# Performance work log

Hardware: AMD Instinct MI355X
Metric: run time of the kernel (lower is better)

The kernel has to match this reference:

```python
import jax, jax.numpy as jnp
import numpy as np

N_NODES = 100000
N_EDGES = 1600000
N_GRAPHS = 256
IN_DIM, HID = 30, 40

def setup_inputs() -> dict:
    key = jax.random.key(0)
    ks = jax.random.split(key, 12)
    x = jax.random.normal(ks[0], (N_NODES, IN_DIM), dtype=jnp.float32)
    edge_index = jax.random.randint(ks[1], (2, N_EDGES), 0, N_NODES, dtype=jnp.int64)
    batch = jnp.sort(jax.random.randint(ks[2], (N_NODES,), 0, N_GRAPHS, dtype=jnp.int64))
    def glorot(k, shape):
        lim = float(np.sqrt(6.0 / (shape[0] + shape[1])))
        return jax.random.uniform(k, shape, dtype=jnp.float32, minval=-lim, maxval=lim)
    return {
        'x': x, 'edge_index': edge_index, 'batch': batch,
        'W1': glorot(ks[3], (IN_DIM, HID)), 'b1': jnp.zeros((HID,), jnp.float32),
        'W2': glorot(ks[4], (HID, HID)),    'b2': jnp.zeros((HID,), jnp.float32),
        'W3': glorot(ks[5], (HID, HID)),    'b3': jnp.zeros((HID,), jnp.float32),
        'lin_w': glorot(ks[6], (HID, 1)),   'lin_b': jnp.zeros((1,), jnp.float32),
    }

def _gcn_layer(x, src, dst, norm, W, b, n_nodes):
    # x: [N, Fin] -> [N, Fout]; fused gather-matmul-scatter form of GCNConv
    h = x @ W                                   # dense transform first (Fout small)
    msg = h[src] * norm[:, None]                # [E+N, Fout] gather + edge scale
    out = jax.ops.segment_sum(msg, dst, num_segments=n_nodes)
    return out + b

def reference(x, edge_index, batch, W1, b1, W2, b2, W3, b3, lin_w, lin_b):
    n = x.shape[0]
    loops = jnp.arange(n, dtype=edge_index.dtype)
    src = jnp.concatenate([edge_index[0], loops])  # add self loops (GCNConv default)
    dst = jnp.concatenate([edge_index[1], loops])
    deg = jax.ops.segment_sum(jnp.ones_like(dst, dtype=x.dtype), dst, num_segments=n)
    dinv = jax.lax.rsqrt(jnp.maximum(deg, 1.0))    # deg >= 1 thanks to self loops
    norm = dinv[src] * dinv[dst]

    h = jax.nn.relu(_gcn_layer(x, src, dst, norm, W1, b1, n))  # dropout inactive (eval)
    h = jax.nn.relu(_gcn_layer(h, src, dst, norm, W2, b2, n))
    h = jax.nn.relu(_gcn_layer(h, src, dst, norm, W3, b3, n))

    # global_mean_pool over graphs
    g_sum = jax.ops.segment_sum(h, batch, num_segments=N_GRAPHS)
    cnt = jax.ops.segment_sum(jnp.ones((n,), h.dtype), batch, num_segments=N_GRAPHS)
    g = g_sum / jnp.maximum(cnt, 1.0)[:, None]
    return g @ lin_w + lin_b                      # [N_GRAPHS, 1]
```

## Files before the change

kernel.cpp:

```cpp
#include <hip/hip_runtime.h>

#define HID 40
#define RBKT 196
#define BSH 9
#define CAP 12288
#define EPB 4096


__device__ inline unsigned pack2_bf16(float a, float b) {
    unsigned ua = __float_as_uint(a);
    unsigned ub = __float_as_uint(b);
    ua = (ua + 0x7fffu + ((ua >> 16) & 1u)) >> 16;
    ub = (ub + 0x7fffu + ((ub >> 16) & 1u)) & 0xffff0000u;
    return ua | ub;
}

__device__ inline void acc8_bf16(float* acc, uint4 v) {
    acc[0] += __uint_as_float(v.x << 16);
    acc[1] += __uint_as_float(v.x & 0xffff0000u);
    acc[2] += __uint_as_float(v.y << 16);
    acc[3] += __uint_as_float(v.y & 0xffff0000u);
    acc[4] += __uint_as_float(v.z << 16);
    acc[5] += __uint_as_float(v.z & 0xffff0000u);
    acc[6] += __uint_as_float(v.w << 16);
    acc[7] += __uint_as_float(v.w & 0xffff0000u);
}

__global__ void clear_kernel(int* __restrict__ bucket_cnt, float* __restrict__ g_sum, int G) {
    int t = blockIdx.x * blockDim.x + threadIdx.x;
    if (t < RBKT) bucket_cnt[t] = 0;
    if (t < G) g_sum[t] = 0.f;
}


__global__ __launch_bounds__(256) void binA_kernel(
        const int* __restrict__ esrc, const int* __restrict__ edst, int E,
        int* __restrict__ bucket_cnt, int* __restrict__ bucket_data) {
    __shared__ int cnt_l[RBKT];
    __shared__ int base_l[RBKT];
    int t = threadIdx.x;
    for (int b = t; b < RBKT; b += 256) cnt_l[b] = 0;
    __syncthreads();
    int e0 = blockIdx.x * EPB;
    int e1 = min(e0 + EPB, E);
    for (int e = e0 + t; e < e1; e += 256) {
        atomicAdd(&cnt_l[edst[e] >> BSH], 1);
    }
    __syncthreads();
    for (int b = t; b < RBKT; b += 256) {
        int c = cnt_l[b];
        base_l[b] = (c > 0) ? atomicAdd(&bucket_cnt[b], c) : 0;
        cnt_l[b] = 0;
    }
    __syncthreads();
    for (int e = e0 + t; e < e1; e += 256) {
        int d = edst[e];
        int s = esrc[e];
        int b = d >> BSH;
        int off = base_l[b] + atomicAdd(&cnt_l[b], 1);
        if (off < CAP) bucket_data[(size_t)b * CAP + off] = (s << BSH) | (d & 511);
    }
}

__global__ void scan_buckets_kernel(const int* __restrict__ cnt, int* __restrict__ base) {
    __shared__ int s[256];
    int t = threadIdx.x;
    int c = (t < RBKT) ? min(cnt[t], CAP) : 0;
    s[t] = c;
    __syncthreads();
    for (int off = 1; off < 256; off <<= 1) {
        int y = (t >= off) ? s[t - off] : 0;
        __syncthreads();
        s[t] += y;
        __syncthreads();
    }
    if (t < RBKT) base[t] = s[t] - c;
    if (t == RBKT - 1) base[RBKT] = s[t];
}

__global__ __launch_bounds__(256) void buildB_kernel(
        const int* __restrict__ bucket_cnt, const int* __restrict__ bucket_base,
        const int* __restrict__ bucket_data,
        int* __restrict__ rowptr, int* __restrict__ mid, int* __restrict__ csr,
        float* __restrict__ dinv, int n, int half) {
    __shared__ int deg_l[512];
    __shared__ int deg_lo[512];
    __shared__ int off_lo[512];
    __shared__ int off_hi[512];
    __shared__ int ps[256];
    int r = blockIdx.x;
    int t = threadIdx.x;
    int cnt = min(bucket_cnt[r], CAP);
    int base = bucket_base[r];
    int node0 = r << BSH;
    int nr = min(512, n - node0);
    for (int i = t; i < 512; i += 256) { deg_l[i] = 0; deg_lo[i] = 0; }
    __syncthreads();
    const int* data = bucket_data + (size_t)r * CAP;
    for (int e = t; e < cnt; e += 256) {
        int v = data[e];
        atomicAdd(&deg_l[v & 511], 1);
        if ((v >> BSH) < half) atomicAdd(&deg_lo[v & 511], 1);
    }
    __syncthreads();
    int a0 = deg_l[2 * t], a1 = deg_l[2 * t + 1];
    ps[t] = a0 + a1;
    __syncthreads();
    for (int off = 1; off < 256; off <<= 1) {
        int y = (t >= off) ? ps[t - off] : 0;
        __syncthreads();
        ps[t] += y;
        __syncthreads();
    }
    int excl = ps[t] - (a0 + a1);
    off_lo[2 * t] = excl;
    off_lo[2 * t + 1] = excl + a0;
    off_hi[2 * t] = excl + deg_lo[2 * t];
    off_hi[2 * t + 1] = excl + a0 + deg_lo[2 * t + 1];
    __syncthreads();
    for (int i = t; i < nr; i += 256) {
        int rp = base + off_lo[i];
        rowptr[node0 + i] = rp;
        mid[node0 + i] = rp + deg_lo[i];
        dinv[node0 + i] = rsqrtf((float)(deg_l[i] + 1));
    }
    if (r == RBKT - 1 && t == 0) rowptr[n] = base + cnt;
    __syncthreads();
    for (int e = t; e < cnt; e += 256) {
        int v = data[e];
        int s = v >> BSH;
        int d = v & 511;
        int p = (s < half) ? atomicAdd(&off_lo[d], 1) : atomicAdd(&off_hi[d], 1);
        csr[base + p] = s;
    }
}


__global__ __launch_bounds__(256) void scale_bf16_kernel(
        const float* __restrict__ x, const float* __restrict__ dinv,
        unsigned* __restrict__ xs, int n) {
    int t = blockIdx.x * blockDim.x + threadIdx.x;
    int i = t >> 4, p = t & 15;
    if (i >= n) return;
    float a = 0.f, b = 0.f;
    if (p < 15) {
        float d = dinv[i];
        a = x[i * 30 + 2 * p] * d;
        b = x[i * 30 + 2 * p + 1] * d;
    }
    xs[(size_t)i * 16 + p] = pack2_bf16(a, b);
}

template <int TPN>
__global__ __launch_bounds__(256) void gather_bf16_kernel(
        const unsigned* __restrict__ xs, const int* __restrict__ rowptr,
        const int* __restrict__ mid, const int* __restrict__ csr,
        const float* __restrict__ dinv, unsigned* __restrict__ gout, int n) {
    int t = blockIdx.x * blockDim.x + threadIdx.x;
    int i = t / TPN;
    int q = t - i * TPN;
    if (i >= n) return;
    const uint4* tab = reinterpret_cast<const uint4*>(xs);
    float acc[8];
    {
        uint4 v = tab[(size_t)i * TPN + q];
        acc[0] = __uint_as_float(v.x << 16);
        acc[1] = __uint_as_float(v.x & 0xffff0000u);
        acc[2] = __uint_as_float(v.y << 16);
        acc[3] = __uint_as_float(v.y & 0xffff0000u);
        acc[4] = __uint_as_float(v.z << 16);
        acc[5] = __uint_as_float(v.z & 0xffff0000u);
        acc[6] = __uint_as_float(v.w << 16);
        acc[7] = __uint_as_float(v.w & 0xffff0000u);
    }
    int e0 = rowptr[i], m = mid[i], e1 = rowptr[i + 1];
    int e = e0;
    for (; e + 4 <= m; e += 4) {
        int s0 = csr[e], s1 = csr[e + 1], s2 = csr[e + 2], s3 = csr[e + 3];
        uint4 v0 = tab[(size_t)s0 * TPN + q];
        uint4 v1 = tab[(size_t)s1 * TPN + q];
        uint4 v2 = tab[(size_t)s2 * TPN + q];
        uint4 v3 = tab[(size_t)s3 * TPN + q];
        acc8_bf16(acc, v0);
        acc8_bf16(acc, v1);
        acc8_bf16(acc, v2);
        acc8_bf16(acc, v3);
    }
    for (; e < m; e++) acc8_bf16(acc, tab[(size_t)csr[e] * TPN + q]);
    for (; e + 4 <= e1; e += 4) {
        int s0 = csr[e], s1 = csr[e + 1], s2 = csr[e + 2], s3 = csr[e + 3];
        uint4 v0 = tab[(size_t)s0 * TPN + q];
        uint4 v1 = tab[(size_t)s1 * TPN + q];
        uint4 v2 = tab[(size_t)s2 * TPN + q];
        uint4 v3 = tab[(size_t)s3 * TPN + q];
        acc8_bf16(acc, v0);
        acc8_bf16(acc, v1);
        acc8_bf16(acc, v2);
        acc8_bf16(acc, v3);
    }
    for (; e < e1; e++) acc8_bf16(acc, tab[(size_t)csr[e] * TPN + q]);
    float d = dinv[i];
    uint4 o;
    o.x = pack2_bf16(acc[0] * d, acc[1] * d);
    o.y = pack2_bf16(acc[2] * d, acc[3] * d);
    o.z = pack2_bf16(acc[4] * d, acc[5] * d);
    o.w = pack2_bf16(acc[6] * d, acc[7] * d);
    reinterpret_cast<uint4*>(gout)[(size_t)i * TPN + q] = o;
}

template <int INF, int RU, bool POOL>
__global__ __launch_bounds__(256) void transform_bf16_kernel(
        const unsigned* __restrict__ tin, const float* __restrict__ W,
        const float* __restrict__ bias, const float* __restrict__ dinv,
        const float* __restrict__ lin_w, const int* __restrict__ batch,
        unsigned* __restrict__ out, float* __restrict__ g_sum, int n) {
    constexpr int OUTF = 40;
    constexpr int OPF  = 10;
    __shared__ float Ws[INF * OUTF];
    __shared__ unsigned tile[64 * (RU + 1)];
    __shared__ float lw[POOL ? OUTF : 1];
    __shared__ float sarr[POOL ? 256 : 1];
    const int tid = threadIdx.x;
    for (int t = tid; t < INF * OUTF; t += 256) Ws[t] = W[t];
    if (POOL && tid < OUTF) lw[tid] = lin_w[tid];
    const int base = blockIdx.x * 64;
    const unsigned* g = tin + (size_t)base * RU;
    const int limit = (n - base) * RU;
    for (int idx = tid; idx < 64 * RU; idx += 256) {
        if (idx < limit) {
            int row = idx / RU, col = idx - row * RU;
            tile[row * (RU + 1) + col] = g[idx];
        }
    }
    __syncthreads();
    const int node_l = tid >> 2, q = tid & 3;
    const int node = base + node_l;
    const bool valid = (node < n);
    if (POOL) sarr[tid] = 0.f;
    if (valid) {
        const unsigned* myrow = &tile[node_l * (RU + 1)];
        float acc[OPF];
        #pragma unroll
        for (int j = 0; j < OPF; j++) acc[j] = 0.f;
        #pragma unroll
        for (int k2 = 0; k2 < INF / 2; k2++) {
            unsigned u = myrow[k2];
            float x0 = __uint_as_float(u << 16);
            float x1 = __uint_as_float(u & 0xffff0000u);
            const float* w0 = &Ws[(2 * k2) * OUTF + q * OPF];
            const float* w1 = &Ws[(2 * k2 + 1) * OUTF + q * OPF];
            #pragma unroll
            for (int j = 0; j < OPF; j++) acc[j] += x0 * w0[j];
            #pragma unroll
            for (int j = 0; j < OPF; j++) acc[j] += x1 * w1[j];
        }
        if (!POOL) {
            float d = dinv[node];
            unsigned* orow = out + (size_t)node * 20 + q * 5;
            #pragma unroll
            for (int j = 0; j < 5; j++) {
                int f = q * OPF + 2 * j;
                float v0 = fmaxf(acc[2 * j] + bias[f], 0.f) * d;
                float v1 = fmaxf(acc[2 * j + 1] + bias[f + 1], 0.f) * d;
                orow[j] = pack2_bf16(v0, v1);
            }
        } else {
            float s = 0.f;
            #pragma unroll
            for (int j = 0; j < OPF; j++) {
                int f = q * OPF + j;
                s += fmaxf(acc[j] + bias[f], 0.f) * lw[f];
            }
            sarr[tid] = s;
        }
    }
    if (POOL) {
        __syncthreads();
        if (tid < 64) {
            float s = sarr[tid * 4] + sarr[tid * 4 + 1] + sarr[tid * 4 + 2] + sarr[tid * 4 + 3];
            int node2 = base + tid;
            bool v2 = (node2 < n);
            int gg = batch[v2 ? node2 : (n - 1)];
            if (!v2) s = 0.f;
            int g0 = __shfl(gg, 0, 64);
            if (__all(gg == g0)) {
                #pragma unroll
                for (int off = 32; off > 0; off >>= 1) s += __shfl_xor(s, off, 64);
                if (tid == 0) atomicAdd(&g_sum[g0], s);
            } else {
                if (v2) atomicAdd(&g_sum[gg], s);
            }
        }
    }
}

__global__ void finalize_kernel(const float* __restrict__ g_sum,
                                const int* __restrict__ batch,
                                const float* __restrict__ lin_b,
                                float* __restrict__ out, int n, int G) {
    int b = blockIdx.x * blockDim.x + threadIdx.x;
    if (b >= G) return;
    int lo = 0, hi = n;
    while (lo < hi) { int m = (lo + hi) >> 1; if (batch[m] < b) lo = m + 1; else hi = m; }
    int lo2 = lo, hi2 = n;
    while (lo2 < hi2) { int m = (lo2 + hi2) >> 1; if (batch[m] < b + 1) lo2 = m + 1; else hi2 = m; }
    int cnt = lo2 - lo;
    out[b] = g_sum[b] / (float)(cnt > 0 ? cnt : 1) + lin_b[0];
}


static inline size_t align_up(size_t v, size_t a) { return (v + a - 1) / a * a; }

extern "C" void kernel_launch(void* const* d_in, const int* in_sizes, int n_in,
                              void* d_out, int out_size, void* d_ws, size_t ws_size,
                              hipStream_t stream) {
    const float* x      = (const float*)d_in[0];
    const int*   esrc   = (const int*)d_in[1];
    const int*   batch  = (const int*)d_in[2];
    const float* W1     = (const float*)d_in[3];
    const float* b1     = (const float*)d_in[4];
    const float* W2     = (const float*)d_in[5];
    const float* b2     = (const float*)d_in[6];
    const float* W3     = (const float*)d_in[7];
    const float* b3     = (const float*)d_in[8];
    const float* lin_w  = (const float*)d_in[9];
    const float* lin_b  = (const float*)d_in[10];
    float* out = (float*)d_out;

    const int n = in_sizes[0] / 30;
    const int E = in_sizes[1] / 2;
    const int G = out_size;
    const int* edst = esrc + E;

    char* w = (char*)d_ws;
    size_t off = 0;
    auto take = [&](size_t bytes) { size_t o = off; off = align_up(off + bytes, 256); return (void*)(w + o); };
    int*      bucket_cnt  = (int*)take((size_t)RBKT * 4);
    int*      bucket_base = (int*)take((size_t)(RBKT + 1) * 4);
    int*      rowptr      = (int*)take((size_t)(n + 1) * 4);
    int*      mid         = (int*)take((size_t)n * 4);
    float*    dinv        = (float*)take((size_t)n * 4);
    int*      csr         = (int*)take((size_t)E * 4);
    float*    g_sum       = (float*)take((size_t)G * 4);
    size_t bd = (size_t)RBKT * CAP * 4;
    size_t x1 = (size_t)n * 16 * 4;
    void* shared_region = take(bd > x1 ? bd : x1);
    int*      bucket_data = (int*)shared_region;
    unsigned* xs1         = (unsigned*)shared_region;
    unsigned* agg         = (unsigned*)take((size_t)n * 20 * 4);
    unsigned* tbA         = (unsigned*)take((size_t)n * 20 * 4);
    unsigned* tbB         = (unsigned*)take((size_t)n * 20 * 4);
    (void)ws_size;

    clear_kernel<<<1, 256, 0, stream>>>(bucket_cnt, g_sum, G);

    binA_kernel<<<(E + EPB - 1) / EPB, 256, 0, stream>>>(esrc, edst, E, bucket_cnt, bucket_data);
    scan_buckets_kernel<<<1, 256, 0, stream>>>(bucket_cnt, bucket_base);
    buildB_kernel<<<RBKT, 256, 0, stream>>>(bucket_cnt, bucket_base, bucket_data,
                                            rowptr, mid, csr, dinv, n, n / 2);

    int nblk64 = (n + 63) / 64;

    scale_bf16_kernel<<<((size_t)n * 16 + 255) / 256, 256, 0, stream>>>(x, dinv, xs1, n);
    gather_bf16_kernel<4><<<((size_t)n * 4 + 255) / 256, 256, 0, stream>>>(
        xs1, rowptr, mid, csr, dinv, agg, n);
    transform_bf16_kernel<30, 16, false><<<nblk64, 256, 0, stream>>>(
        agg, W1, b1, dinv, nullptr, nullptr, tbA, nullptr, n);
    gather_bf16_kernel<5><<<((size_t)n * 5 + 255) / 256, 256, 0, stream>>>(
        tbA, rowptr, mid, csr, dinv, agg, n);
    transform_bf16_kernel<40, 20, false><<<nblk64, 256, 0, stream>>>(
        agg, W2, b2, dinv, nullptr, nullptr, tbB, nullptr, n);
    gather_bf16_kernel<5><<<((size_t)n * 5 + 255) / 256, 256, 0, stream>>>(
        tbB, rowptr, mid, csr, dinv, agg, n);
    transform_bf16_kernel<40, 20, true><<<nblk64, 256, 0, stream>>>(
        agg, W3, b3, dinv, lin_w, batch, nullptr, g_sum, n);

    finalize_kernel<<<1, 256, 0, stream>>>(g_sum, batch, lin_b, out, n, G);
}
```

Before: 216.6 us.

## Restructure transform kernel to one node per thread with output-slice blocks

The dense transform kernel now gives each thread a whole node and half of the output features (20), splitting the two output halves across paired blocks of 256 nodes. Weights are read directly from global memory (uniform across the wavefront, so scalar/broadcast loads) instead of staging them in shared memory, and the pooling reduction uses per-wavefront shuffles without a shared-memory pass. This cuts shared-memory weight traffic and block-level syncs. In exchange each input tile is loaded twice (once per slice), register pressure rises, and the inner k loop is no longer forced to unroll.

```diff
diff --git a/kernel.cpp b/kernel.cpp
--- a/kernel.cpp
+++ b/kernel.cpp
@@ -209,46 +209,42 @@
 }
 
 template <int INF, int RU, bool POOL>
-__global__ __launch_bounds__(256) void transform_bf16_kernel(
+__global__ __launch_bounds__(256) void transform_v2_kernel(
         const unsigned* __restrict__ tin, const float* __restrict__ W,
         const float* __restrict__ bias, const float* __restrict__ dinv,
         const float* __restrict__ lin_w, const int* __restrict__ batch,
         unsigned* __restrict__ out, float* __restrict__ g_sum, int n) {
     constexpr int OUTF = 40;
-    constexpr int OPF  = 10;
-    __shared__ float Ws[INF * OUTF];
-    __shared__ unsigned tile[64 * (RU + 1)];
-    __shared__ float lw[POOL ? OUTF : 1];
-    __shared__ float sarr[POOL ? 256 : 1];
+    constexpr int OPF  = 20;
+    __shared__ unsigned tile[256 * (RU + 1)];
     const int tid = threadIdx.x;
-    for (int t = tid; t < INF * OUTF; t += 256) Ws[t] = W[t];
-    if (POOL && tid < OUTF) lw[tid] = lin_w[tid];
-    const int base = blockIdx.x * 64;
+    const int nodeblk = blockIdx.x >> 1;
+    const int slice = blockIdx.x & 1;
+    const int q0 = slice * OPF;
+    const int base = nodeblk * 256;
     const unsigned* g = tin + (size_t)base * RU;
-    const int limit = (n - base) * RU;
-    for (int idx = tid; idx < 64 * RU; idx += 256) {
+    const int limit = (min(256, n - base)) * RU;
+    for (int idx = tid; idx < 256 * RU; idx += 256) {
         if (idx < limit) {
-            int row = idx / RU, col = idx - row * RU;
-            tile[row * (RU + 1) + col] = g[idx];
+            int r = idx / RU, c = idx - r * RU;
+            tile[r * (RU + 1) + c] = g[idx];
         }
     }
     __syncthreads();
-    const int node_l = tid >> 2, q = tid & 3;
-    const int node = base + node_l;
+    const int node = base + tid;
     const bool valid = (node < n);
-    if (POOL) sarr[tid] = 0.f;
+    float s = 0.f;
     if (valid) {
-        const unsigned* myrow = &tile[node_l * (RU + 1)];
+        const unsigned* myrow = &tile[tid * (RU + 1)];
         float acc[OPF];
         #pragma unroll
         for (int j = 0; j < OPF; j++) acc[j] = 0.f;
-        #pragma unroll
         for (int k2 = 0; k2 < INF / 2; k2++) {
             unsigned u = myrow[k2];
             float x0 = __uint_as_float(u << 16);
             float x1 = __uint_as_float(u & 0xffff0000u);
-            const float* w0 = &Ws[(2 * k2) * OUTF + q * OPF];
-            const float* w1 = &Ws[(2 * k2 + 1) * OUTF + q * OPF];
+            const float* w0 = &W[(2 * k2) * OUTF + q0];
+            const float* w1 = &W[(2 * k2 + 1) * OUTF + q0];
             #pragma unroll
             for (int j = 0; j < OPF; j++) acc[j] += x0 * w0[j];
             #pragma unroll
@@ -256,40 +252,30 @@
         }
         if (!POOL) {
             float d = dinv[node];
-            unsigned* orow = out + (size_t)node * 20 + q * 5;
-            #pragma unroll
-            for (int j = 0; j < 5; j++) {
-                int f = q * OPF + 2 * j;
-                float v0 = fmaxf(acc[2 * j] + bias[f], 0.f) * d;
-                float v1 = fmaxf(acc[2 * j + 1] + bias[f + 1], 0.f) * d;
+            unsigned* orow = out + (size_t)node * 20 + slice * 10;
+            #pragma unroll
+            for (int j = 0; j < OPF / 2; j++) {
+                float v0 = fmaxf(acc[2 * j] + bias[q0 + 2 * j], 0.f) * d;
+                float v1 = fmaxf(acc[2 * j + 1] + bias[q0 + 2 * j + 1], 0.f) * d;
                 orow[j] = pack2_bf16(v0, v1);
             }
         } else {
-            float s = 0.f;
             #pragma unroll
             for (int j = 0; j < OPF; j++) {
-                int f = q * OPF + j;
-                s += fmaxf(acc[j] + bias[f], 0.f) * lw[f];
+                s += fmaxf(acc[j] + bias[q0 + j], 0.f) * lin_w[q0 + j];
             }
-            sarr[tid] = s;
         }
     }
     if (POOL) {
-        __syncthreads();
-        if (tid < 64) {
-            float s = sarr[tid * 4] + sarr[tid * 4 + 1] + sarr[tid * 4 + 2] + sarr[tid * 4 + 3];
-            int node2 = base + tid;
-            bool v2 = (node2 < n);
-            int gg = batch[v2 ? node2 : (n - 1)];
-            if (!v2) s = 0.f;
-            int g0 = __shfl(gg, 0, 64);
-            if (__all(gg == g0)) {
-                #pragma unroll
-                for (int off = 32; off > 0; off >>= 1) s += __shfl_xor(s, off, 64);
-                if (tid == 0) atomicAdd(&g_sum[g0], s);
-            } else {
-                if (v2) atomicAdd(&g_sum[gg], s);
-            }
+        int gg = batch[valid ? node : (n - 1)];
+        if (!valid) s = 0.f;
+        int g0 = __shfl(gg, 0, 64);
+        if (__all(gg == g0)) {
+            #pragma unroll
+            for (int off = 32; off > 0; off >>= 1) s += __shfl_xor(s, off, 64);
+            if ((tid & 63) == 0) atomicAdd(&g_sum[g0], s);
+        } else {
+            if (valid) atomicAdd(&g_sum[gg], s);
         }
     }
 }
@@ -359,20 +345,20 @@
     buildB_kernel<<<RBKT, 256, 0, stream>>>(bucket_cnt, bucket_base, bucket_data,
                                             rowptr, mid, csr, dinv, n, n / 2);
 
-    int nblk64 = (n + 63) / 64;
+    int nblk256 = (n + 255) / 256;
 
     scale_bf16_kernel<<<((size_t)n * 16 + 255) / 256, 256, 0, stream>>>(x, dinv, xs1, n);
     gather_bf16_kernel<4><<<((size_t)n * 4 + 255) / 256, 256, 0, stream>>>(
         xs1, rowptr, mid, csr, dinv, agg, n);
-    transform_bf16_kernel<30, 16, false><<<nblk64, 256, 0, stream>>>(
+    transform_v2_kernel<30, 16, false><<<nblk256 * 2, 256, 0, stream>>>(
         agg, W1, b1, dinv, nullptr, nullptr, tbA, nullptr, n);
     gather_bf16_kernel<5><<<((size_t)n * 5 + 255) / 256, 256, 0, stream>>>(
         tbA, rowptr, mid, csr, dinv, agg, n);
-    transform_bf16_kernel<40, 20, false><<<nblk64, 256, 0, stream>>>(
+    transform_v2_kernel<40, 20, false><<<nblk256 * 2, 256, 0, stream>>>(
         agg, W2, b2, dinv, nullptr, nullptr, tbB, nullptr, n);
     gather_bf16_kernel<5><<<((size_t)n * 5 + 255) / 256, 256, 0, stream>>>(
         tbB, rowptr, mid, csr, dinv, agg, n);
-    transform_bf16_kernel<40, 20, true><<<nblk64, 256, 0, stream>>>(
+    transform_v2_kernel<40, 20, true><<<nblk256 * 2, 256, 0, stream>>>(
         agg, W3, b3, dinv, lin_w, batch, nullptr, g_sum, n);
 
     finalize_kernel<<<1, 256, 0, stream>>>(g_sum, batch, lin_b, out, n, G);
```

New measurement: 244.9 us. 13.1% more time.
